# Optimization experiments

Measured on AMD Instinct MI355X. Metric: run time of the kernel, lower is better.

The kernel has to match this reference:

```python
import jax, jax.numpy as jnp
import numpy as np

BATCH = 4096
DIM = 512
TEMP = 0.5
EPS = 1e-8


def setup_inputs() -> dict:
    key = jax.random.key(0)
    k1, k2 = jax.random.split(key)
    z_i = jax.random.normal(k1, (BATCH, DIM), dtype=jnp.float32)
    z_j = jax.random.normal(k2, (BATCH, DIM), dtype=jnp.float32)
    return {"z_i": z_i, "z_j": z_j}


def reference(z_i, z_j):
    N = z_i.shape[0]
    temperature = jnp.asarray(TEMP, z_i.dtype)
    z = jnp.concatenate([z_i, z_j], axis=0)  # [2N, D]
    # cosine similarity = (x . y) / max(||x||*||y||, eps), as torch CosineSimilarity
    norms = jnp.sqrt(jnp.sum(z * z, axis=-1, keepdims=True))  # [2N, 1]
    dots = z @ z.T                                            # [2N, 2N]
    denom = jnp.maximum(norms * norms.T, EPS)
    sim = dots / denom / temperature                          # [2N, 2N]

    idx = jnp.arange(2 * N)
    # positive pair: offset +N / -N diagonals == partner index (i+N) mod 2N
    pos = sim[idx, (idx + N) % (2 * N)]                       # [2N]
    # CE with label 0 over logits [pos, negatives]: the full candidate set per
    # row is every sim entry except the self-diagonal (positive included once).
    masked = jnp.where(jnp.eye(2 * N, dtype=bool), -jnp.inf, sim)
    lse = jax.nn.logsumexp(masked, axis=1)                    # [2N]
    loss = jnp.sum(lse - pos) / (2 * N)
    return loss
```

## Files before the change

kernel.cpp:

```cpp
#include <hip/hip_runtime.h>


#define NROWS 8192
#define HALF_N 4096
#define KD 512
#define TILE 128
#define BK 128
#define NT (NROWS / TILE)

typedef unsigned char u8;
typedef __attribute__((ext_vector_type(4))) int i32x4;
typedef __attribute__((ext_vector_type(8))) int i32x8;
typedef __attribute__((ext_vector_type(4))) float f32x4;

__device__ inline void load16_to_lds(const u8* g, u8* l) {
  __builtin_amdgcn_global_load_lds((const __attribute__((address_space(1))) void*)g,
                                   (__attribute__((address_space(3))) void*)l,
                                   16, 0, 0);
}

__global__ __launch_bounds__(256) void nt_normalize(const float* __restrict__ zi,
                                                    const float* __restrict__ zj,
                                                    u8* __restrict__ zq,
                                                    float* __restrict__ rowsum,
                                                    float* __restrict__ possum,
                                                    float* __restrict__ out) {
  const int t = threadIdx.x;
  if (t < 4) rowsum[blockIdx.x * 4 + t] = 0.f;
  if (blockIdx.x == 0 && t == 4) { possum[0] = 0.f; out[0] = 0.f; }

  const int wave = t >> 6, lane = t & 63;
  const int row = blockIdx.x * 4 + wave;
  const float* src = (row < HALF_N) ? (zi + (size_t)row * KD)
                                    : (zj + (size_t)(row - HALF_N) * KD);
  const float4 v0 = ((const float4*)src)[lane * 2];
  const float4 v1 = ((const float4*)src)[lane * 2 + 1];
  float ss = v0.x * v0.x + v0.y * v0.y + v0.z * v0.z + v0.w * v0.w +
             v1.x * v1.x + v1.y * v1.y + v1.z * v1.z + v1.w * v1.w;
#pragma unroll
  for (int m = 1; m < 64; m <<= 1) ss += __shfl_xor(ss, m);
  const float inv = rsqrtf(ss);
  int lo = __builtin_amdgcn_cvt_pk_fp8_f32(v0.x * inv, v0.y * inv, 0, false);
  lo = __builtin_amdgcn_cvt_pk_fp8_f32(v0.z * inv, v0.w * inv, lo, true);
  int hi = __builtin_amdgcn_cvt_pk_fp8_f32(v1.x * inv, v1.y * inv, 0, false);
  hi = __builtin_amdgcn_cvt_pk_fp8_f32(v1.z * inv, v1.w * inv, hi, true);
  ((int2*)(zq + (size_t)row * KD))[lane] = make_int2(lo, hi);
}

__global__ __launch_bounds__(256) void nt_gemm(const u8* __restrict__ zq,
                                               float* __restrict__ rowsum,
                                               float* __restrict__ possum) {
  __shared__ __attribute__((aligned(16))) u8 lA[TILE * BK];
  __shared__ __attribute__((aligned(16))) u8 lB[TILE * BK];
  __shared__ float lrow[TILE];
  __shared__ float lcol[TILE];

  const int bid = blockIdx.x;
  int tm = (int)((float)(2 * NT + 1) * 0.5f -
                 sqrtf((float)(2 * NT + 1) * (float)(2 * NT + 1) * 0.25f - 2.0f * (float)bid));
  if (tm < 0) tm = 0;
  if (tm > NT - 1) tm = NT - 1;
  while ((tm + 1) * NT - ((tm + 1) * tm) / 2 <= bid) ++tm;
  while (tm * NT - (tm * (tm - 1)) / 2 > bid) --tm;
  const int tn = tm + (bid - (tm * NT - (tm * (tm - 1)) / 2));
  const bool diag = (tm == tn);
  const bool isPos = (tn - tm == 32);

  const int t = threadIdx.x;
  const int wave = t >> 6, lane = t & 63;
  const int wm = wave >> 1, wn = wave & 1;
  const int c16 = lane & 15, quad = lane >> 4;

  const int rowA = tm * TILE, rowB = tn * TILE;

  f32x4 acc[4][4] = {};

  const u8* Bt = diag ? lA : lB;
  const int q2 = quad * 2;

  for (int k0 = 0; k0 < KD; k0 += BK) {
    __syncthreads();
#pragma unroll
    for (int it = 0; it < 4; ++it) {
      const int chunk = it * 256 + t;
      const int r = chunk >> 3, cpos = chunk & 7;
      const int c = cpos ^ (r & 7);
      u8* dstA = &lA[(it * 256 + wave * 64) * 16];
      load16_to_lds(&zq[(size_t)(rowA + r) * KD + k0 + c * 16], dstA);
      if (!diag) {
        u8* dstB = &lB[(it * 256 + wave * 64) * 16];
        load16_to_lds(&zq[(size_t)(rowB + r) * KD + k0 + c * 16], dstB);
      }
    }
    __syncthreads();

    i32x8 bg[4];
#pragma unroll
    for (int ni = 0; ni < 4; ++ni) {
      const int rB = wn * 64 + ni * 16 + c16;
      const i32x4 bl = *(const i32x4*)&Bt[(rB * 8 + (q2 ^ (rB & 7))) * 16];
      const i32x4 bh = *(const i32x4*)&Bt[(rB * 8 + ((q2 + 1) ^ (rB & 7))) * 16];
      bg[ni] = (i32x8){bl[0], bl[1], bl[2], bl[3], bh[0], bh[1], bh[2], bh[3]};
    }
#pragma unroll
    for (int mi = 0; mi < 4; ++mi) {
      const int rA = wm * 64 + mi * 16 + c16;
      const i32x4 al = *(const i32x4*)&lA[(rA * 8 + (q2 ^ (rA & 7))) * 16];
      const i32x4 ah = *(const i32x4*)&lA[(rA * 8 + ((q2 + 1) ^ (rA & 7))) * 16];
      const i32x8 af = (i32x8){al[0], al[1], al[2], al[3], ah[0], ah[1], ah[2], ah[3]};
#pragma unroll
      for (int ni = 0; ni < 4; ++ni)
        acc[mi][ni] = __builtin_amdgcn_mfma_scale_f32_16x16x128_f8f6f4(
            af, bg[ni], acc[mi][ni],
            0, 0,
            0, 0x7F7F7F7F,
            0, 0x7F7F7F7F);
    }
  }

  const bool ownDiag = (quad == (c16 >> 2));
  const int rdiag = c16 & 3;

  if (isPos && wm == wn) {
    float p = 0.f;
    if (ownDiag) {
#pragma unroll
      for (int mi = 0; mi < 4; ++mi) p += acc[mi][mi][rdiag];
    }
#pragma unroll
    for (int m = 1; m < 64; m <<= 1) p += __shfl_xor(p, m);
    if (lane == 0) atomicAdd(possum, 4.0f * p);
  }

#pragma unroll
  for (int mi = 0; mi < 4; ++mi)
#pragma unroll
    for (int ni = 0; ni < 4; ++ni)
#pragma unroll
      for (int r = 0; r < 4; ++r)
        acc[mi][ni][r] = __expf(2.0f * acc[mi][ni][r]);

  if (diag && wm == wn && ownDiag) {
#pragma unroll
    for (int mi = 0; mi < 4; ++mi) acc[mi][mi][rdiag] = 0.f;
  }

  if (t < TILE) { lrow[t] = 0.f; lcol[t] = 0.f; }
  __syncthreads();

#pragma unroll
  for (int mi = 0; mi < 4; ++mi) {
#pragma unroll
    for (int r = 0; r < 4; ++r) {
      float e = acc[mi][0][r] + acc[mi][1][r] + acc[mi][2][r] + acc[mi][3][r];
      e += __shfl_xor(e, 1);
      e += __shfl_xor(e, 2);
      e += __shfl_xor(e, 4);
      e += __shfl_xor(e, 8);
      if (c16 == 0) atomicAdd(&lrow[wm * 64 + mi * 16 + quad * 4 + r], e);
    }
  }
  if (!diag) {
#pragma unroll
    for (int ni = 0; ni < 4; ++ni) {
      float g = 0.f;
#pragma unroll
      for (int mi = 0; mi < 4; ++mi)
#pragma unroll
        for (int r = 0; r < 4; ++r) g += acc[mi][ni][r];
      g += __shfl_xor(g, 16);
      g += __shfl_xor(g, 32);
      if (quad == 0) atomicAdd(&lcol[wn * 64 + ni * 16 + c16], g);
    }
  }
  __syncthreads();
  if (t < TILE) {
    atomicAdd(&rowsum[rowA + t], lrow[t]);
    if (!diag) atomicAdd(&rowsum[rowB + t], lcol[t]);
  }
}

__global__ __launch_bounds__(256) void nt_finalize(const float* __restrict__ rowsum,
                                                   const float* __restrict__ possum,
                                                   float* __restrict__ out) {
  const int t = threadIdx.x;
  const int i = blockIdx.x * 256 + t;
  float v = logf(rowsum[i]);
#pragma unroll
  for (int m = 1; m < 64; m <<= 1) v += __shfl_xor(v, m);
  __shared__ float bsum[4];
  if ((t & 63) == 0) bsum[t >> 6] = v;
  __syncthreads();
  if (t == 0) {
    float s = bsum[0] + bsum[1] + bsum[2] + bsum[3];
    if (blockIdx.x == 0) s -= possum[0];
    atomicAdd(out, s * (1.0f / NROWS));
  }
}

extern "C" void kernel_launch(void* const* d_in, const int* in_sizes, int n_in,
                              void* d_out, int out_size, void* d_ws, size_t ws_size,
                              hipStream_t stream) {
  const float* zi = (const float*)d_in[0];
  const float* zj = (const float*)d_in[1];
  float* out = (float*)d_out;

  u8* zq = (u8*)d_ws;
  float* rowsum = (float*)((char*)d_ws + (size_t)NROWS * KD);
  float* possum = rowsum + NROWS;

  nt_normalize<<<NROWS / 4, 256, 0, stream>>>(zi, zj, zq, rowsum, possum, out);
  nt_gemm<<<NT * (NT + 1) / 2, 256, 0, stream>>>(zq, rowsum, possum);
  nt_finalize<<<NROWS / 256, 256, 0, stream>>>(rowsum, possum, out);
}
```

Baseline: 109.8 us.

## Double-buffer LDS tiles with async prefetch and remap block order

```diff
diff --git a/kernel.cpp b/kernel.cpp
--- a/kernel.cpp
+++ b/kernel.cpp
@@ -7,6 +7,7 @@
 #define TILE 128
 #define BK 128
 #define NT (NROWS / TILE)
+#define NBLK (NT * (NT + 1) / 2)
 
 typedef unsigned char u8;
 typedef __attribute__((ext_vector_type(4))) int i32x4;
@@ -50,12 +51,13 @@
 __global__ __launch_bounds__(256) void nt_gemm(const u8* __restrict__ zq,
                                                float* __restrict__ rowsum,
                                                float* __restrict__ possum) {
-  __shared__ __attribute__((aligned(16))) u8 lA[TILE * BK];
-  __shared__ __attribute__((aligned(16))) u8 lB[TILE * BK];
+  __shared__ __attribute__((aligned(16))) u8 lA[2][TILE * BK];
+  __shared__ __attribute__((aligned(16))) u8 lB[2][TILE * BK];
   __shared__ float lrow[TILE];
   __shared__ float lcol[TILE];
 
-  const int bid = blockIdx.x;
+  const int bid = (blockIdx.x & 7) * (NBLK / 8) + (blockIdx.x >> 3);
+
   int tm = (int)((float)(2 * NT + 1) * 0.5f -
                  sqrtf((float)(2 * NT + 1) * (float)(2 * NT + 1) * 0.25f - 2.0f * (float)bid));
   if (tm < 0) tm = 0;
@@ -70,52 +72,73 @@
   const int wave = t >> 6, lane = t & 63;
   const int wm = wave >> 1, wn = wave & 1;
   const int c16 = lane & 15, quad = lane >> 4;
+  const int q2 = quad * 2;
 
   const int rowA = tm * TILE, rowB = tn * TILE;
 
   f32x4 acc[4][4] = {};
 
-  const u8* Bt = diag ? lA : lB;
-  const int q2 = quad * 2;
-
-  for (int k0 = 0; k0 < KD; k0 += BK) {
-    __syncthreads();
+  auto stage = [&](int k0, int buf) {
 #pragma unroll
     for (int it = 0; it < 4; ++it) {
       const int chunk = it * 256 + t;
       const int r = chunk >> 3, cpos = chunk & 7;
       const int c = cpos ^ (r & 7);
-      u8* dstA = &lA[(it * 256 + wave * 64) * 16];
+      u8* dstA = &lA[buf][(it * 256 + wave * 64) * 16];
+      u8* dstB = &lB[buf][(it * 256 + wave * 64) * 16];
       load16_to_lds(&zq[(size_t)(rowA + r) * KD + k0 + c * 16], dstA);
-      if (!diag) {
-        u8* dstB = &lB[(it * 256 + wave * 64) * 16];
-        load16_to_lds(&zq[(size_t)(rowB + r) * KD + k0 + c * 16], dstB);
-      }
-    }
-    __syncthreads();
-
-    i32x8 bg[4];
+      load16_to_lds(&zq[(size_t)(rowB + r) * KD + k0 + c * 16], dstB);
+    }
+  };
+
+  stage(0, 0);
+
+#pragma unroll
+  for (int k = 0; k < 4; ++k) {
+    const int cur = k & 1;
+    if (k < 3) {
+      stage((k + 1) * BK, cur ^ 1);
+      asm volatile("s_waitcnt vmcnt(8)" ::: "memory");
+    } else {
+      asm volatile("s_waitcnt vmcnt(0)" ::: "memory");
+    }
+    __builtin_amdgcn_s_barrier();
+    __builtin_amdgcn_sched_barrier(0);
+
+    const u8* Ab = lA[cur];
+    const u8* Bb = lB[cur];
+
+    i32x8 bg[4], ag[4];
 #pragma unroll
     for (int ni = 0; ni < 4; ++ni) {
       const int rB = wn * 64 + ni * 16 + c16;
-      const i32x4 bl = *(const i32x4*)&Bt[(rB * 8 + (q2 ^ (rB & 7))) * 16];
-      const i32x4 bh = *(const i32x4*)&Bt[(rB * 8 + ((q2 + 1) ^ (rB & 7))) * 16];
+      const i32x4 bl = *(const i32x4*)&Bb[(rB * 8 + (q2 ^ (rB & 7))) * 16];
+      const i32x4 bh = *(const i32x4*)&Bb[(rB * 8 + ((q2 + 1) ^ (rB & 7))) * 16];
       bg[ni] = (i32x8){bl[0], bl[1], bl[2], bl[3], bh[0], bh[1], bh[2], bh[3]};
     }
 #pragma unroll
     for (int mi = 0; mi < 4; ++mi) {
       const int rA = wm * 64 + mi * 16 + c16;
-      const i32x4 al = *(const i32x4*)&lA[(rA * 8 + (q2 ^ (rA & 7))) * 16];
-      const i32x4 ah = *(const i32x4*)&lA[(rA * 8 + ((q2 + 1) ^ (rA & 7))) * 16];
-      const i32x8 af = (i32x8){al[0], al[1], al[2], al[3], ah[0], ah[1], ah[2], ah[3]};
+      const i32x4 al = *(const i32x4*)&Ab[(rA * 8 + (q2 ^ (rA & 7))) * 16];
+      const i32x4 ah = *(const i32x4*)&Ab[(rA * 8 + ((q2 + 1) ^ (rA & 7))) * 16];
+      ag[mi] = (i32x8){al[0], al[1], al[2], al[3], ah[0], ah[1], ah[2], ah[3]};
+    }
+
+    __builtin_amdgcn_s_setprio(1);
+#pragma unroll
+    for (int mi = 0; mi < 4; ++mi)
 #pragma unroll
       for (int ni = 0; ni < 4; ++ni)
         acc[mi][ni] = __builtin_amdgcn_mfma_scale_f32_16x16x128_f8f6f4(
-            af, bg[ni], acc[mi][ni],
+            ag[mi], bg[ni], acc[mi][ni],
             0, 0,
             0, 0x7F7F7F7F,
             0, 0x7F7F7F7F);
-    }
+    __builtin_amdgcn_s_setprio(0);
+
+    asm volatile("s_waitcnt lgkmcnt(0)" ::: "memory");
+    __builtin_amdgcn_s_barrier();
+    __builtin_amdgcn_sched_barrier(0);
   }
 
   const bool ownDiag = (quad == (c16 >> 2));
```

Measured after the change: 110.4 us. No clear change (+0.5%).

## Replace global rowsum atomics with per-tile partial buffer and remap block order

Applied to the files above, without the earlier changes.

```diff
diff --git a/kernel.cpp b/kernel.cpp
--- a/kernel.cpp
+++ b/kernel.cpp
@@ -7,6 +7,7 @@
 #define TILE 128
 #define BK 128
 #define NT (NROWS / TILE)
+#define NBLK (NT * (NT + 1) / 2)
 
 typedef unsigned char u8;
 typedef __attribute__((ext_vector_type(4))) int i32x4;
@@ -22,12 +23,10 @@
 __global__ __launch_bounds__(256) void nt_normalize(const float* __restrict__ zi,
                                                     const float* __restrict__ zj,
                                                     u8* __restrict__ zq,
-                                                    float* __restrict__ rowsum,
                                                     float* __restrict__ possum,
                                                     float* __restrict__ out) {
   const int t = threadIdx.x;
-  if (t < 4) rowsum[blockIdx.x * 4 + t] = 0.f;
-  if (blockIdx.x == 0 && t == 4) { possum[0] = 0.f; out[0] = 0.f; }
+  if (blockIdx.x == 0 && t == 0) { possum[0] = 0.f; out[0] = 0.f; }
 
   const int wave = t >> 6, lane = t & 63;
   const int row = blockIdx.x * 4 + wave;
@@ -48,14 +47,15 @@
 }
 
 __global__ __launch_bounds__(256) void nt_gemm(const u8* __restrict__ zq,
-                                               float* __restrict__ rowsum,
+                                               float* __restrict__ P,
                                                float* __restrict__ possum) {
   __shared__ __attribute__((aligned(16))) u8 lA[TILE * BK];
   __shared__ __attribute__((aligned(16))) u8 lB[TILE * BK];
   __shared__ float lrow[TILE];
   __shared__ float lcol[TILE];
 
-  const int bid = blockIdx.x;
+  const int bid = (blockIdx.x & 7) * (NBLK / 8) + (blockIdx.x >> 3);
+
   int tm = (int)((float)(2 * NT + 1) * 0.5f -
                  sqrtf((float)(2 * NT + 1) * (float)(2 * NT + 1) * 0.25f - 2.0f * (float)bid));
   if (tm < 0) tm = 0;
@@ -70,13 +70,13 @@
   const int wave = t >> 6, lane = t & 63;
   const int wm = wave >> 1, wn = wave & 1;
   const int c16 = lane & 15, quad = lane >> 4;
+  const int q2 = quad * 2;
 
   const int rowA = tm * TILE, rowB = tn * TILE;
 
   f32x4 acc[4][4] = {};
 
   const u8* Bt = diag ? lA : lB;
-  const int q2 = quad * 2;
 
   for (int k0 = 0; k0 < KD; k0 += BK) {
     __syncthreads();
@@ -175,17 +175,25 @@
   }
   __syncthreads();
   if (t < TILE) {
-    atomicAdd(&rowsum[rowA + t], lrow[t]);
-    if (!diag) atomicAdd(&rowsum[rowB + t], lcol[t]);
-  }
-}
-
-__global__ __launch_bounds__(256) void nt_finalize(const float* __restrict__ rowsum,
+    P[(size_t)tn * NROWS + rowA + t] = lrow[t];
+    if (!diag) P[(size_t)tm * NROWS + rowB + t] = lcol[t];
+  }
+}
+
+__global__ __launch_bounds__(256) void nt_finalize(const float* __restrict__ P,
                                                    const float* __restrict__ possum,
                                                    float* __restrict__ out) {
   const int t = threadIdx.x;
   const int i = blockIdx.x * 256 + t;
-  float v = logf(rowsum[i]);
+  float s0 = 0.f, s1 = 0.f, s2 = 0.f, s3 = 0.f;
+#pragma unroll
+  for (int s = 0; s < NT; s += 4) {
+    s0 += P[(size_t)(s + 0) * NROWS + i];
+    s1 += P[(size_t)(s + 1) * NROWS + i];
+    s2 += P[(size_t)(s + 2) * NROWS + i];
+    s3 += P[(size_t)(s + 3) * NROWS + i];
+  }
+  float v = logf((s0 + s1) + (s2 + s3));
 #pragma unroll
   for (int m = 1; m < 64; m <<= 1) v += __shfl_xor(v, m);
   __shared__ float bsum[4];
@@ -206,10 +214,10 @@
   float* out = (float*)d_out;
 
   u8* zq = (u8*)d_ws;
-  float* rowsum = (float*)((char*)d_ws + (size_t)NROWS * KD);
-  float* possum = rowsum + NROWS;
-
-  nt_normalize<<<NROWS / 4, 256, 0, stream>>>(zi, zj, zq, rowsum, possum, out);
-  nt_gemm<<<NT * (NT + 1) / 2, 256, 0, stream>>>(zq, rowsum, possum);
-  nt_finalize<<<NROWS / 256, 256, 0, stream>>>(rowsum, possum, out);
-}
+  float* P = (float*)((char*)d_ws + (size_t)NROWS * KD);
+  float* possum = P + (size_t)NT * NROWS;
+
+  nt_normalize<<<NROWS / 4, 256, 0, stream>>>(zi, zj, zq, possum, out);
+  nt_gemm<<<NBLK, 256, 0, stream>>>(zq, P, possum);
+  nt_finalize<<<NROWS / 256, 256, 0, stream>>>(P, possum, out);
+}
```

After: 126.8 us. +15.4%, slower.

## Enlarge GEMM tile to 256x256 with 512 threads and XCD-aware block remap

Applied to the files above, without the earlier changes.

```diff
diff --git a/kernel.cpp b/kernel.cpp
--- a/kernel.cpp
+++ b/kernel.cpp
@@ -4,9 +4,10 @@
 #define NROWS 8192
 #define HALF_N 4096
 #define KD 512
-#define TILE 128
+#define BM 256
 #define BK 128
-#define NT (NROWS / TILE)
+#define NT2 (NROWS / BM)
+#define NBLK (NT2 * (NT2 + 1) / 2)
 
 typedef unsigned char u8;
 typedef __attribute__((ext_vector_type(4))) int i32x4;
@@ -47,48 +48,47 @@
   ((int2*)(zq + (size_t)row * KD))[lane] = make_int2(lo, hi);
 }
 
-__global__ __launch_bounds__(256) void nt_gemm(const u8* __restrict__ zq,
-                                               float* __restrict__ rowsum,
-                                               float* __restrict__ possum) {
-  __shared__ __attribute__((aligned(16))) u8 lA[TILE * BK];
-  __shared__ __attribute__((aligned(16))) u8 lB[TILE * BK];
-  __shared__ float lrow[TILE];
-  __shared__ float lcol[TILE];
-
-  const int bid = blockIdx.x;
-  int tm = (int)((float)(2 * NT + 1) * 0.5f -
-                 sqrtf((float)(2 * NT + 1) * (float)(2 * NT + 1) * 0.25f - 2.0f * (float)bid));
+__global__ __launch_bounds__(512, 2) void nt_gemm(const u8* __restrict__ zq,
+                                                  float* __restrict__ rowsum,
+                                                  float* __restrict__ possum) {
+  __shared__ __attribute__((aligned(16))) u8 lA[BM * BK];
+  __shared__ __attribute__((aligned(16))) u8 lB[BM * BK];
+
+  const int bid = (blockIdx.x & 7) * (NBLK / 8) + (blockIdx.x >> 3);
+
+  int tm = (int)((float)(2 * NT2 + 1) * 0.5f -
+                 sqrtf((float)(2 * NT2 + 1) * (float)(2 * NT2 + 1) * 0.25f - 2.0f * (float)bid));
   if (tm < 0) tm = 0;
-  if (tm > NT - 1) tm = NT - 1;
-  while ((tm + 1) * NT - ((tm + 1) * tm) / 2 <= bid) ++tm;
-  while (tm * NT - (tm * (tm - 1)) / 2 > bid) --tm;
-  const int tn = tm + (bid - (tm * NT - (tm * (tm - 1)) / 2));
+  if (tm > NT2 - 1) tm = NT2 - 1;
+  while ((tm + 1) * NT2 - ((tm + 1) * tm) / 2 <= bid) ++tm;
+  while (tm * NT2 - (tm * (tm - 1)) / 2 > bid) --tm;
+  const int tn = tm + (bid - (tm * NT2 - (tm * (tm - 1)) / 2));
   const bool diag = (tm == tn);
-  const bool isPos = (tn - tm == 32);
+  const bool isPos = (tn - tm == (HALF_N / BM));
 
   const int t = threadIdx.x;
   const int wave = t >> 6, lane = t & 63;
-  const int wm = wave >> 1, wn = wave & 1;
+  const int wm = wave >> 2, wn = wave & 3;
   const int c16 = lane & 15, quad = lane >> 4;
-
-  const int rowA = tm * TILE, rowB = tn * TILE;
-
-  f32x4 acc[4][4] = {};
+  const int q2 = quad * 2;
+
+  const int rowA = tm * BM, rowB = tn * BM;
+
+  f32x4 acc[8][4] = {};
 
   const u8* Bt = diag ? lA : lB;
-  const int q2 = quad * 2;
 
   for (int k0 = 0; k0 < KD; k0 += BK) {
     __syncthreads();
 #pragma unroll
     for (int it = 0; it < 4; ++it) {
-      const int chunk = it * 256 + t;
+      const int chunk = it * 512 + t;
       const int r = chunk >> 3, cpos = chunk & 7;
       const int c = cpos ^ (r & 7);
-      u8* dstA = &lA[(it * 256 + wave * 64) * 16];
+      u8* dstA = &lA[(it * 512 + wave * 64) * 16];
       load16_to_lds(&zq[(size_t)(rowA + r) * KD + k0 + c * 16], dstA);
       if (!diag) {
-        u8* dstB = &lB[(it * 256 + wave * 64) * 16];
+        u8* dstB = &lB[(it * 512 + wave * 64) * 16];
         load16_to_lds(&zq[(size_t)(rowB + r) * KD + k0 + c * 16], dstB);
       }
     }
@@ -102,9 +102,10 @@
       const i32x4 bh = *(const i32x4*)&Bt[(rB * 8 + ((q2 + 1) ^ (rB & 7))) * 16];
       bg[ni] = (i32x8){bl[0], bl[1], bl[2], bl[3], bh[0], bh[1], bh[2], bh[3]};
     }
-#pragma unroll
-    for (int mi = 0; mi < 4; ++mi) {
-      const int rA = wm * 64 + mi * 16 + c16;
+    __builtin_amdgcn_s_setprio(1);
+#pragma unroll
+    for (int mi = 0; mi < 8; ++mi) {
+      const int rA = wm * 128 + mi * 16 + c16;
       const i32x4 al = *(const i32x4*)&lA[(rA * 8 + (q2 ^ (rA & 7))) * 16];
       const i32x4 ah = *(const i32x4*)&lA[(rA * 8 + ((q2 + 1) ^ (rA & 7))) * 16];
       const i32x8 af = (i32x8){al[0], al[1], al[2], al[3], ah[0], ah[1], ah[2], ah[3]};
@@ -116,16 +117,23 @@
             0, 0x7F7F7F7F,
             0, 0x7F7F7F7F);
     }
-  }
+    __builtin_amdgcn_s_setprio(0);
+  }
+  __syncthreads();
+
+  float* lrow = (float*)lA;
+  float* lcol = lrow + BM;
 
   const bool ownDiag = (quad == (c16 >> 2));
   const int rdiag = c16 & 3;
-
-  if (isPos && wm == wn) {
+  const bool diagWave = ((wn >> 1) == wm);
+  const int miOff = (wn & 1) * 4;
+
+  if (isPos && diagWave) {
     float p = 0.f;
     if (ownDiag) {
 #pragma unroll
-      for (int mi = 0; mi < 4; ++mi) p += acc[mi][mi][rdiag];
+      for (int ni = 0; ni < 4; ++ni) p += acc[miOff + ni][ni][rdiag];
     }
 #pragma unroll
     for (int m = 1; m < 64; m <<= 1) p += __shfl_xor(p, m);
@@ -133,23 +141,23 @@
   }
 
 #pragma unroll
-  for (int mi = 0; mi < 4; ++mi)
+  for (int mi = 0; mi < 8; ++mi)
 #pragma unroll
     for (int ni = 0; ni < 4; ++ni)
 #pragma unroll
       for (int r = 0; r < 4; ++r)
         acc[mi][ni][r] = __expf(2.0f * acc[mi][ni][r]);
 
-  if (diag && wm == wn && ownDiag) {
-#pragma unroll
-    for (int mi = 0; mi < 4; ++mi) acc[mi][mi][rdiag] = 0.f;
-  }
-
-  if (t < TILE) { lrow[t] = 0.f; lcol[t] = 0.f; }
-  __syncthreads();
-
-#pragma unroll
-  for (int mi = 0; mi < 4; ++mi) {
+  if (diag && diagWave && ownDiag) {
+#pragma unroll
+    for (int ni = 0; ni < 4; ++ni) acc[miOff + ni][ni][rdiag] = 0.f;
+  }
+
+  if (t < BM) { lrow[t] = 0.f; lcol[t] = 0.f; }
+  __syncthreads();
+
+#pragma unroll
+  for (int mi = 0; mi < 8; ++mi) {
 #pragma unroll
     for (int r = 0; r < 4; ++r) {
       float e = acc[mi][0][r] + acc[mi][1][r] + acc[mi][2][r] + acc[mi][3][r];
@@ -157,7 +165,7 @@
       e += __shfl_xor(e, 2);
       e += __shfl_xor(e, 4);
       e += __shfl_xor(e, 8);
-      if (c16 == 0) atomicAdd(&lrow[wm * 64 + mi * 16 + quad * 4 + r], e);
+      if (c16 == 0) atomicAdd(&lrow[wm * 128 + mi * 16 + quad * 4 + r], e);
     }
   }
   if (!diag) {
@@ -165,7 +173,7 @@
     for (int ni = 0; ni < 4; ++ni) {
       float g = 0.f;
 #pragma unroll
-      for (int mi = 0; mi < 4; ++mi)
+      for (int mi = 0; mi < 8; ++mi)
 #pragma unroll
         for (int r = 0; r < 4; ++r) g += acc[mi][ni][r];
       g += __shfl_xor(g, 16);
@@ -174,7 +182,7 @@
     }
   }
   __syncthreads();
-  if (t < TILE) {
+  if (t < BM) {
     atomicAdd(&rowsum[rowA + t], lrow[t]);
     if (!diag) atomicAdd(&rowsum[rowB + t], lcol[t]);
   }
@@ -210,6 +218,6 @@
   float* possum = rowsum + NROWS;
 
   nt_normalize<<<NROWS / 4, 256, 0, stream>>>(zi, zj, zq, rowsum, possum, out);
-  nt_gemm<<<NT * (NT + 1) / 2, 256, 0, stream>>>(zq, rowsum, possum);
+  nt_gemm<<<NBLK, 512, 0, stream>>>(zq, rowsum, possum);
   nt_finalize<<<NROWS / 256, 256, 0, stream>>>(rowsum, possum, out);
 }
```

After: 381.8 us. 3.48x slower.
